# Kernel optimization log

Measured on AMD Instinct MI355X. Metric: run time of the kernel, lower is better.

The kernel has to match this reference:

```python
import jax, jax.numpy as jnp
import numpy as np
from jax import lax

B, T, C = 4, 1024, 1024
H, HEAD = 16, 64            # n_head, head size (K == V == HEAD)
TM_DIM, TD_DIM = 32, 64     # TIME_MIX_EXTRA_DIM, W_MIX_EXTRA_DIM
N_LAYER, LAYER_ID = 24, 12
EPS = 1e-5
HEAD_DIV = 8.0              # head_size_divisor


def setup_inputs() -> dict:
    key = jax.random.key(0)
    ks = jax.random.split(key, 10)
    r1 = 1.0 - LAYER_ID / N_LAYER          # ratio_1_to_almost0
    r0 = LAYER_ID / max(N_LAYER - 1, 1)    # ratio_0_to_1
    ddd = np.arange(C, dtype=np.float64) / C
    x_maa = (1.0 - ddd ** r1).astype(np.float32)
    r_maa = (1.0 - ddd ** (0.5 * r1)).astype(np.float32)
    v_maa = (1.0 - (ddd ** r1 + 0.3 * r0)).astype(np.float32)
    n = np.arange(H * HEAD, dtype=np.float64)
    denom = max(H * HEAD - 1, 1)
    time_decay = (-6.0 + 5.0 * (n / denom) ** (0.7 + 1.3 * r0)).reshape(H, HEAD).astype(np.float32)
    zig = (((np.arange(H * HEAD) + 1) % 3) - 1) * 0.1
    time_first = (r0 * (1.0 - n / denom) + zig).reshape(H, HEAD).astype(np.float32)

    def unif(k, shape, s=0.01):
        return jax.random.uniform(k, shape, jnp.float32, -s, s)

    return {
        "x": jax.random.normal(ks[0], (B, T, C), jnp.float32),
        "x_maa": jnp.asarray(x_maa),
        "w_maa": jnp.asarray(x_maa),
        "k_maa": jnp.asarray(x_maa),
        "v_maa": jnp.asarray(v_maa),
        "r_maa": jnp.asarray(r_maa),
        "g_maa": jnp.asarray(r_maa),
        "tm_w1": unif(ks[1], (C, 5 * TM_DIM)),
        "tm_w2": unif(ks[2], (5, TM_DIM, C)),
        "td_w1": unif(ks[3], (C, TD_DIM)),
        "td_w2": unif(ks[4], (TD_DIM, C)),
        "time_decay": jnp.asarray(time_decay),
        "time_first": jnp.asarray(time_first),
        "Wr": jax.random.normal(ks[5], (C, H * HEAD), jnp.float32) * 0.02,
        "Wk": jax.random.normal(ks[6], (C, H * HEAD), jnp.float32) * 0.02,
        "Wv": jax.random.normal(ks[7], (C, H * HEAD), jnp.float32) * 0.02,
        "Wg": jax.random.normal(ks[8], (C, H * HEAD), jnp.float32) * 0.02,
        "Wo": jax.random.normal(ks[9], (H * HEAD, C), jnp.float32) * 0.02,
        "ln_w": jnp.ones((H * HEAD,), jnp.float32),
        "ln_b": jnp.zeros((H * HEAD,), jnp.float32),
    }


def reference(x, x_maa, w_maa, k_maa, v_maa, r_maa, g_maa,
              tm_w1, tm_w2, td_w1, td_w2, time_decay, time_first,
              Wr, Wk, Wv, Wg, Wo, ln_w, ln_b):
    B, T, C = x.shape
    H, K = time_decay.shape
    V = Wv.shape[1] // H
    # token shift: sx = x_{t-1} - x_t (zero-padded at t=0)
    sx = jnp.concatenate([jnp.zeros_like(x[:, :1]), x[:, :-1]], axis=1) - x
    # data-dependent token-mix LoRA: 5 mixing deltas
    mix = jnp.tanh((x + sx * x_maa) @ tm_w1).reshape(B, T, 5, TM_DIM)
    mix = jnp.einsum('btfd,fdc->fbtc', mix, tm_w2)  # [5,B,T,C]
    mw, mk, mv, mr, mg = mix
    wx = x + sx * (w_maa + mw)
    kx = x + sx * (k_maa + mk)
    vx = x + sx * (v_maa + mv)
    rx = x + sx * (r_maa + mr)
    gx = x + sx * (g_maa + mg)
    r = (rx @ Wr).reshape(B, T, H, K)
    k = (kx @ Wk).reshape(B, T, H, K)
    v = (vx @ Wv).reshape(B, T, H, V)
    g = jax.nn.silu(gx @ Wg)                         # [B,T,H*V]
    # data-dependent decay via LoRA, then double-exp squash into (0,1)
    w = time_decay[None, None] + (jnp.tanh(wx @ td_w1) @ td_w2).reshape(B, T, H, K)
    w = jnp.exp(-jnp.exp(w))                         # [B,T,H,K]
    u = time_first                                   # [H,K]

    def step(s, inp):
        rt, kt, vt, wt = inp                         # [B,H,K],[B,H,K],[B,H,V],[B,H,K]
        kv = kt[..., None] * vt[..., None, :]        # [B,H,K,V] outer product
        y = jnp.einsum('bhk,bhkv->bhv', rt, s + u[None, :, :, None] * kv)
        return wt[..., None] * s + kv, y

    s0 = jnp.zeros((B, H, K, V), x.dtype)
    xs = (jnp.moveaxis(r, 1, 0), jnp.moveaxis(k, 1, 0),
          jnp.moveaxis(v, 1, 0), jnp.moveaxis(w, 1, 0))
    _, ys = lax.scan(step, s0, xs)                   # ys: [T,B,H,V]
    out = jnp.moveaxis(ys, 0, 1).reshape(B, T, H, V) / HEAD_DIV
    # GroupNorm with n_kv_head groups over dim_v channels -> per-head norm
    mu = out.mean(-1, keepdims=True)
    var = out.var(-1, keepdims=True)
    out = ((out - mu) * lax.rsqrt(var + EPS)).reshape(B, T, H * V) * ln_w + ln_b
    return (out * g) @ Wo
```

## Files before the change

kernel.cpp:

```cpp
#include <hip/hip_runtime.h>
#include <hip/hip_bf16.h>
#include <math.h>
#include <stdint.h>

constexpr int Bn = 4, Tn = 1024, Cn = 1024, Hn = 16;
constexpr int BT = Bn * Tn;
constexpr long long BTC = (long long)BT * Cn;
constexpr int CL = 64;
constexpr int NC = Tn / CL;

typedef __bf16 bf16x8_t __attribute__((ext_vector_type(8)));
typedef float f32x4_t __attribute__((ext_vector_type(4)));
typedef unsigned short us8_t __attribute__((ext_vector_type(8)));

__device__ __forceinline__ unsigned short f2bf_bits(float v) {
    __hip_bfloat16 h = __float2bfloat16(v);
    return *reinterpret_cast<unsigned short*>(&h);
}
__device__ __forceinline__ float bfbits2f(unsigned short u) {
    unsigned int x = (unsigned int)u << 16;
    return __uint_as_float(x);
}

__device__ __forceinline__ void gload16(const void* g, void* l) {
    auto const* gp = reinterpret_cast<const unsigned int __attribute__((address_space(1)))*>(
        reinterpret_cast<uintptr_t>(g));
    auto* lp = reinterpret_cast<unsigned int __attribute__((address_space(3)))*>(
        reinterpret_cast<uintptr_t>(l));
    __builtin_amdgcn_global_load_lds(gp, lp, 16, 0, 0);
}

__global__ __launch_bounds__(256) void transp8(const float* __restrict__ W0,
                                               const float* __restrict__ W1,
                                               const float* __restrict__ W2,
                                               const float* __restrict__ W3,
                                               const float* __restrict__ W4,
                                               const float* __restrict__ W5,
                                               const float* __restrict__ W6,
                                               const float* __restrict__ W7,
                                               __hip_bfloat16* __restrict__ T0,
                                               __hip_bfloat16* __restrict__ T1,
                                               __hip_bfloat16* __restrict__ T2,
                                               __hip_bfloat16* __restrict__ T3,
                                               __hip_bfloat16* __restrict__ T4,
                                               __hip_bfloat16* __restrict__ T5,
                                               __hip_bfloat16* __restrict__ T6,
                                               __hip_bfloat16* __restrict__ T7) {
    int z = blockIdx.z;
    const float* W;
    __hip_bfloat16* Wt;
    int R, Cc;
    if (z < 5) {
        W = (z == 0) ? W0 : (z == 1) ? W1 : (z == 2) ? W2 : (z == 3) ? W3 : W4;
        Wt = (z == 0) ? T0 : (z == 1) ? T1 : (z == 2) ? T2 : (z == 3) ? T3 : T4;
        R = Cn; Cc = Cn;
    } else if (z == 5) {
        if (blockIdx.x >= 5) return;
        W = W5; Wt = T5; R = Cn; Cc = 160;
    } else if (z == 6) {
        if (blockIdx.y >= 5) return;
        W = W6; Wt = T6; R = 160; Cc = Cn;
    } else {
        if (blockIdx.y >= 2) return;
        W = W7; Wt = T7; R = 64; Cc = Cn;
    }
    __shared__ float tile[32][33];
    int c0 = blockIdx.x * 32, r0 = blockIdx.y * 32;
    int tx = threadIdx.x & 31, ty = threadIdx.x >> 5;
    #pragma unroll
    for (int i = 0; i < 4; i++)
        tile[ty + 8 * i][tx] = W[(size_t)(r0 + ty + 8 * i) * Cc + c0 + tx];
    __syncthreads();
    #pragma unroll
    for (int i = 0; i < 4; i++)
        Wt[(size_t)(c0 + ty + 8 * i) * R + r0 + tx] = __float2bfloat16(tile[tx][ty + 8 * i]);
}

template <int KS>
__global__ __launch_bounds__(256) void gemm_f32_splitk(const float* __restrict__ A,
                                                       const float* __restrict__ Bm,
                                                       float* __restrict__ part,
                                                       int M, int N, int K) {
    __shared__ float As[16][64];
    __shared__ float Bs[16][64];
    int tid = threadIdx.x;
    int kp = blockIdx.x;
    int m0 = blockIdx.y * 64;
    int kbeg = kp * (K / KS), kend = kbeg + K / KS;
    int tx = tid & 15, ty = tid >> 4;
    int ar = tid >> 2, ac = (tid & 3) * 4;
    int br = tid >> 4, bc = (tid & 15) * 4;
    float acc[4][4] = {};

    for (int k0 = kbeg; k0 < kend; k0 += 16) {
        float4 av = *reinterpret_cast<const float4*>(A + (size_t)(m0 + ar) * K + k0 + ac);
        As[ac + 0][ar] = av.x; As[ac + 1][ar] = av.y;
        As[ac + 2][ar] = av.z; As[ac + 3][ar] = av.w;
        *reinterpret_cast<float4*>(&Bs[br][bc]) =
            *reinterpret_cast<const float4*>(Bm + (size_t)(k0 + br) * N + bc);
        __syncthreads();
        #pragma unroll
        for (int kk = 0; kk < 16; kk++) {
            float4 a4 = *reinterpret_cast<const float4*>(&As[kk][ty * 4]);
            float4 b4 = *reinterpret_cast<const float4*>(&Bs[kk][tx * 4]);
            float aa[4] = {a4.x, a4.y, a4.z, a4.w};
            float bb[4] = {b4.x, b4.y, b4.z, b4.w};
            #pragma unroll
            for (int i = 0; i < 4; i++)
                #pragma unroll
                for (int j = 0; j < 4; j++)
                    acc[i][j] = fmaf(aa[i], bb[j], acc[i][j]);
        }
        __syncthreads();
    }
    #pragma unroll
    for (int i = 0; i < 4; i++) {
        int row = m0 + ty * 4 + i;
        #pragma unroll
        for (int j = 0; j < 4; j++)
            part[((size_t)kp * M + row) * N + tx * 4 + j] = acc[i][j];
    }
}

template <int KS>
__global__ __launch_bounds__(256) void splitk_reduce_tanh_bf(const float* __restrict__ part,
                                                             __hip_bfloat16* __restrict__ outp,
                                                             int total, size_t stride) {
    int i = blockIdx.x * 256 + threadIdx.x;
    if (i >= total) return;
    float s = 0.f;
    #pragma unroll
    for (int kp = 0; kp < KS; kp++) s += part[kp * stride + i];
    outp[i] = __float2bfloat16(tanhf(s));
}

template <int KS>
__global__ __launch_bounds__(256) void gemm_mfma_sk(const float* __restrict__ x,
                                                    const float* __restrict__ x_maa,
                                                    const __hip_bfloat16* __restrict__ Bt,
                                                    float* __restrict__ part,
                                                    int M, int N, int K) {
    __shared__ alignas(16) unsigned short As[64 * 64];
    __shared__ alignas(16) unsigned short Bs[128 * 64];
    int tid = threadIdx.x;
    int m0 = blockIdx.y * 64, n0 = blockIdx.x * 128;
    int kp = blockIdx.z;
    int kbeg = kp * (K / KS), kend = kbeg + K / KS;
    int wave = tid >> 6, lane = tid & 63;
    int wm = (wave & 1) * 32, wn = (wave >> 1) * 64;
    int l15 = lane & 15, l4 = lane >> 4;
    f32x4_t acc[2][4] = {};

    for (int k0 = kbeg; k0 < kend; k0 += 64) {
        #pragma unroll
        for (int p = 0; p < 2; p++) {
            int cch = tid + p * 256;
            int row = cch >> 3, slot = cch & 7;
            int s2 = slot ^ (row & 7);
            int gr = m0 + row;
            int t = gr & (Tn - 1);
            size_t gx = (size_t)gr * Cn + k0 + slot * 8;
            float4 xa0 = *reinterpret_cast<const float4*>(x + gx);
            float4 xa1 = *reinterpret_cast<const float4*>(x + gx + 4);
            float4 xp0 = make_float4(0.f, 0.f, 0.f, 0.f), xp1 = xp0;
            if (t > 0) {
                xp0 = *reinterpret_cast<const float4*>(x + gx - Cn);
                xp1 = *reinterpret_cast<const float4*>(x + gx - Cn + 4);
            }
            float4 ma0 = *reinterpret_cast<const float4*>(x_maa + k0 + slot * 8);
            float4 ma1 = *reinterpret_cast<const float4*>(x_maa + k0 + slot * 8 + 4);
            ushort4 o0, o1;
            o0.x = f2bf_bits(xa0.x + (xp0.x - xa0.x) * ma0.x);
            o0.y = f2bf_bits(xa0.y + (xp0.y - xa0.y) * ma0.y);
            o0.z = f2bf_bits(xa0.z + (xp0.z - xa0.z) * ma0.z);
            o0.w = f2bf_bits(xa0.w + (xp0.w - xa0.w) * ma0.w);
            o1.x = f2bf_bits(xa1.x + (xp1.x - xa1.x) * ma1.x);
            o1.y = f2bf_bits(xa1.y + (xp1.y - xa1.y) * ma1.y);
            o1.z = f2bf_bits(xa1.z + (xp1.z - xa1.z) * ma1.z);
            o1.w = f2bf_bits(xa1.w + (xp1.w - xa1.w) * ma1.w);
            *reinterpret_cast<ushort4*>(&As[row * 64 + s2 * 8]) = o0;
            *reinterpret_cast<ushort4*>(&As[row * 64 + s2 * 8 + 4]) = o1;
        }
        #pragma unroll
        for (int p = 0; p < 4; p++) {
            int cch = tid + p * 256;
            int row = cch >> 3, slot = cch & 7;
            int s2 = slot ^ (row & 7);
            int rowg = n0 + row; if (rowg > N - 1) rowg = N - 1;
            *reinterpret_cast<us8_t*>(&Bs[row * 64 + s2 * 8]) =
                *reinterpret_cast<const us8_t*>(&Bt[(size_t)rowg * K + k0 + slot * 8]);
        }
        __syncthreads();
        #pragma unroll
        for (int kw = 0; kw < 2; kw++) {
            int slot = kw * 4 + l4;
            bf16x8_t af[2], bfr[4];
            #pragma unroll
            for (int f = 0; f < 2; f++) {
                int ar = wm + f * 16 + l15;
                af[f] = *reinterpret_cast<const bf16x8_t*>(&As[ar * 64 + (slot ^ (ar & 7)) * 8]);
            }
            #pragma unroll
            for (int f = 0; f < 4; f++) {
                int br = wn + f * 16 + l15;
                bfr[f] = *reinterpret_cast<const bf16x8_t*>(&Bs[br * 64 + (slot ^ (br & 7)) * 8]);
            }
            #pragma unroll
            for (int i = 0; i < 2; i++)
                #pragma unroll
                for (int j = 0; j < 4; j++)
                    acc[i][j] = __builtin_amdgcn_mfma_f32_16x16x32_bf16(af[i], bfr[j], acc[i][j], 0, 0, 0);
        }
        __syncthreads();
    }

    #pragma unroll
    for (int i = 0; i < 2; i++) {
        int rbase = m0 + wm + i * 16 + l4 * 4;
        #pragma unroll
        for (int j = 0; j < 4; j++) {
            int col = n0 + wn + j * 16 + l15;
            if (col < N) {
                #pragma unroll
                for (int q = 0; q < 4; q++)
                    part[((size_t)kp * M + rbase + q) * N + col] = acc[i][j][q];
            }
        }
    }
}

__global__ __launch_bounds__(256) void gemm_mfma_decay(const __hip_bfloat16* __restrict__ A,
                                                       const __hip_bfloat16* __restrict__ Bt,
                                                       const float* __restrict__ extra,
                                                       float* __restrict__ Cout,
                                                       int M, int N) {
    __shared__ alignas(16) unsigned short As[64 * 64];
    __shared__ alignas(16) unsigned short Bs[128 * 64];
    int tid = threadIdx.x;
    int m0 = blockIdx.x * 64, n0 = blockIdx.y * 128;
    int wave = tid >> 6, lane = tid & 63;
    int wm = (wave & 1) * 32, wn = (wave >> 1) * 64;
    int l15 = lane & 15, l4 = lane >> 4;
    int lrow = lane >> 3, ls2 = lane & 7;
    f32x4_t acc[2][4] = {};

    #pragma unroll
    for (int ci = 0; ci < 2; ci++) {
        int r0 = wave * 16 + ci * 8;
        int row = r0 + lrow;
        int gs = ls2 ^ (row & 7);
        gload16(&A[(size_t)(m0 + row) * 64 + gs * 8], &As[r0 * 64]);
    }
    #pragma unroll
    for (int ci = 0; ci < 4; ci++) {
        int r0 = wave * 32 + ci * 8;
        int row = r0 + lrow;
        int gs = ls2 ^ (row & 7);
        gload16(&Bt[(size_t)(n0 + row) * 64 + gs * 8], &Bs[r0 * 64]);
    }
    __syncthreads();
    #pragma unroll
    for (int kw = 0; kw < 2; kw++) {
        int slot = kw * 4 + l4;
        bf16x8_t af[2], bfr[4];
        #pragma unroll
        for (int f = 0; f < 2; f++) {
            int ar = wm + f * 16 + l15;
            af[f] = *reinterpret_cast<const bf16x8_t*>(&As[ar * 64 + (slot ^ (ar & 7)) * 8]);
        }
        #pragma unroll
        for (int f = 0; f < 4; f++) {
            int br = wn + f * 16 + l15;
            bfr[f] = *reinterpret_cast<const bf16x8_t*>(&Bs[br * 64 + (slot ^ (br & 7)) * 8]);
        }
        #pragma unroll
        for (int i = 0; i < 2; i++)
            #pragma unroll
            for (int j = 0; j < 4; j++)
                acc[i][j] = __builtin_amdgcn_mfma_f32_16x16x32_bf16(af[i], bfr[j], acc[i][j], 0, 0, 0);
    }

    #pragma unroll
    for (int i = 0; i < 2; i++) {
        int rbase = m0 + wm + i * 16 + l4 * 4;
        #pragma unroll
        for (int j = 0; j < 4; j++) {
            int col = n0 + wn + j * 16 + l15;
            float ex = extra[col];
            #pragma unroll
            for (int q = 0; q < 4; q++)
                Cout[(size_t)(rbase + q) * N + col] = -expf(ex + acc[i][j][q]);
        }
    }
}

__global__ __launch_bounds__(256) void dmix_gemm(const __hip_bfloat16* __restrict__ A,
                                                 const __hip_bfloat16* __restrict__ W2T,
                                                 const float* __restrict__ x,
                                                 const float* __restrict__ wmaa,
                                                 const float* __restrict__ kmaa,
                                                 const float* __restrict__ vmaa,
                                                 const float* __restrict__ rmaa,
                                                 const float* __restrict__ gmaa,
                                                 float* __restrict__ wx,
                                                 __hip_bfloat16* __restrict__ kxb,
                                                 __hip_bfloat16* __restrict__ vxb,
                                                 __hip_bfloat16* __restrict__ rxb,
                                                 __hip_bfloat16* __restrict__ gxb) {
    __shared__ alignas(16) unsigned short As[64 * 32];
    __shared__ alignas(16) unsigned short Bs[128 * 32];
    int tid = threadIdx.x;
    int m0 = blockIdx.x * 64, n0 = blockIdx.y * 128;
    int f  = blockIdx.z;
    int wave = tid >> 6, lane = tid & 63;
    int wm = (wave & 1) * 32, wn = (wave >> 1) * 64;
    int l15 = lane & 15, l4 = lane >> 4;
    int lrow2 = lane >> 2, ls = lane & 3;
    f32x4_t acc[2][4] = {};

    {
        int row = wave * 16 + lrow2;
        int gs = ls ^ (row & 3);
        gload16(&A[(size_t)(m0 + row) * 160 + f * 32 + gs * 8], &As[(wave * 16) * 32]);
    }
    #pragma unroll
    for (int ci = 0; ci < 2; ci++) {
        int r0 = wave * 32 + ci * 16;
        int row = r0 + lrow2;
        int gs = ls ^ (row & 3);
        gload16(&W2T[(size_t)(n0 + row) * 160 + f * 32 + gs * 8], &Bs[r0 * 32]);
    }
    __syncthreads();
    bf16x8_t af[2], bfr[4];
    #pragma unroll
    for (int i = 0; i < 2; i++) {
        int ar = wm + i * 16 + l15;
        af[i] = *reinterpret_cast<const bf16x8_t*>(&As[ar * 32 + ((l4 ^ (ar & 3)) * 8)]);
    }
    #pragma unroll
    for (int j = 0; j < 4; j++) {
        int br = wn + j * 16 + l15;
        bfr[j] = *reinterpret_cast<const bf16x8_t*>(&Bs[br * 32 + ((l4 ^ (br & 3)) * 8)]);
    }
    #pragma unroll
    for (int i = 0; i < 2; i++)
        #pragma unroll
        for (int j = 0; j < 4; j++)
            acc[i][j] = __builtin_amdgcn_mfma_f32_16x16x32_bf16(af[i], bfr[j], acc[i][j], 0, 0, 0);

    const float* maa = (f == 0) ? wmaa : (f == 1) ? kmaa : (f == 2) ? vmaa
                     : (f == 3) ? rmaa : gmaa;
    __hip_bfloat16* dstb = (f == 1) ? kxb : (f == 2) ? vxb : (f == 3) ? rxb : gxb;
    #pragma unroll
    for (int i = 0; i < 2; i++) {
        int rbase = m0 + wm + i * 16 + l4 * 4;
        #pragma unroll
        for (int j = 0; j < 4; j++) {
            int col = n0 + wn + j * 16 + l15;
            float mv = maa[col];
            #pragma unroll
            for (int q = 0; q < 4; q++) {
                int row = rbase + q;
                int t = row & (Tn - 1);
                size_t o = (size_t)row * Cn + col;
                float xv = x[o];
                float xp = (t > 0) ? x[o - Cn] : 0.f;
                float val = xv + (xp - xv) * (mv + acc[i][j][q]);
                if (f == 0) wx[o] = val;
                else        dstb[o] = __float2bfloat16(val);
            }
        }
    }
}

__global__ __launch_bounds__(256) void gemm_qkvg(const __hip_bfloat16* __restrict__ A0,
                                                 const __hip_bfloat16* __restrict__ A1,
                                                 const __hip_bfloat16* __restrict__ A2,
                                                 const __hip_bfloat16* __restrict__ A3,
                                                 const __hip_bfloat16* __restrict__ B0,
                                                 const __hip_bfloat16* __restrict__ B1,
                                                 const __hip_bfloat16* __restrict__ B2,
                                                 const __hip_bfloat16* __restrict__ B3,
                                                 __hip_bfloat16* __restrict__ C0,
                                                 __hip_bfloat16* __restrict__ C1,
                                                 __hip_bfloat16* __restrict__ C2,
                                                 __hip_bfloat16* __restrict__ C3,
                                                 int M, int N, int K) {
    int g = blockIdx.z;
    const __hip_bfloat16* A  = (g == 0) ? A0 : (g == 1) ? A1 : (g == 2) ? A2 : A3;
    const __hip_bfloat16* Bt = (g == 0) ? B0 : (g == 1) ? B1 : (g == 2) ? B2 : B3;
    __hip_bfloat16* Co = (g == 0) ? C0 : (g == 1) ? C1 : (g == 2) ? C2 : C3;
    __shared__ alignas(16) unsigned short As[64 * 64];
    __shared__ alignas(16) unsigned short Bs[128 * 64];
    int tid = threadIdx.x;
    int m0 = blockIdx.x * 64, n0 = blockIdx.y * 128;
    int wave = tid >> 6, lane = tid & 63;
    int wm = (wave & 1) * 32, wn = (wave >> 1) * 64;
    int l15 = lane & 15, l4 = lane >> 4;
    int lrow = lane >> 3, ls2 = lane & 7;
    f32x4_t acc[2][4] = {};

    for (int k0 = 0; k0 < K; k0 += 64) {
        #pragma unroll
        for (int ci = 0; ci < 2; ci++) {
            int r0 = wave * 16 + ci * 8;
            int row = r0 + lrow;
            int gs = ls2 ^ (row & 7);
            gload16(&A[(size_t)(m0 + row) * K + k0 + gs * 8], &As[r0 * 64]);
        }
        #pragma unroll
        for (int ci = 0; ci < 4; ci++) {
            int r0 = wave * 32 + ci * 8;
            int row = r0 + lrow;
            int gs = ls2 ^ (row & 7);
            gload16(&Bt[(size_t)(n0 + row) * K + k0 + gs * 8], &Bs[r0 * 64]);
        }
        __syncthreads();
        #pragma unroll
        for (int kw = 0; kw < 2; kw++) {
            int slot = kw * 4 + l4;
            bf16x8_t af[2], bfr[4];
            #pragma unroll
            for (int f = 0; f < 2; f++) {
                int ar = wm + f * 16 + l15;
                af[f] = *reinterpret_cast<const bf16x8_t*>(&As[ar * 64 + (slot ^ (ar & 7)) * 8]);
            }
            #pragma unroll
            for (int f = 0; f < 4; f++) {
                int br = wn + f * 16 + l15;
                bfr[f] = *reinterpret_cast<const bf16x8_t*>(&Bs[br * 64 + (slot ^ (br & 7)) * 8]);
            }
            #pragma unroll
            for (int i = 0; i < 2; i++)
                #pragma unroll
                for (int j = 0; j < 4; j++)
                    acc[i][j] = __builtin_amdgcn_mfma_f32_16x16x32_bf16(af[i], bfr[j], acc[i][j], 0, 0, 0);
        }
        __syncthreads();
    }

    #pragma unroll
    for (int i = 0; i < 2; i++) {
        int rbase = m0 + wm + i * 16 + l4 * 4;
        #pragma unroll
        for (int j = 0; j < 4; j++) {
            int col = n0 + wn + j * 16 + l15;
            #pragma unroll
            for (int q = 0; q < 4; q++) {
                float v = acc[i][j][q];
                if (g == 3) v = v / (1.f + expf(-v));
                Co[(size_t)(rbase + q) * N + col] = __float2bfloat16(v);
            }
        }
    }
}

__global__ __launch_bounds__(256) void gemm_mfma_gl(const __hip_bfloat16* __restrict__ A,
                                                    const __hip_bfloat16* __restrict__ Bt,
                                                    float* __restrict__ Cout,
                                                    int M, int N, int K) {
    __shared__ alignas(16) unsigned short As[64 * 64];
    __shared__ alignas(16) unsigned short Bs[128 * 64];
    int tid = threadIdx.x;
    int m0 = blockIdx.x * 64, n0 = blockIdx.y * 128;
    int wave = tid >> 6, lane = tid & 63;
    int wm = (wave & 1) * 32, wn = (wave >> 1) * 64;
    int l15 = lane & 15, l4 = lane >> 4;
    int lrow = lane >> 3, ls2 = lane & 7;
    f32x4_t acc[2][4] = {};

    for (int k0 = 0; k0 < K; k0 += 64) {
        #pragma unroll
        for (int ci = 0; ci < 2; ci++) {
            int r0 = wave * 16 + ci * 8;
            int row = r0 + lrow;
            int gs = ls2 ^ (row & 7);
            gload16(&A[(size_t)(m0 + row) * K + k0 + gs * 8], &As[r0 * 64]);
        }
        #pragma unroll
        for (int ci = 0; ci < 4; ci++) {
            int r0 = wave * 32 + ci * 8;
            int row = r0 + lrow;
            int gs = ls2 ^ (row & 7);
            gload16(&Bt[(size_t)(n0 + row) * K + k0 + gs * 8], &Bs[r0 * 64]);
        }
        __syncthreads();
        #pragma unroll
        for (int kw = 0; kw < 2; kw++) {
            int slot = kw * 4 + l4;
            bf16x8_t af[2], bfr[4];
            #pragma unroll
            for (int f = 0; f < 2; f++) {
                int ar = wm + f * 16 + l15;
                af[f] = *reinterpret_cast<const bf16x8_t*>(&As[ar * 64 + (slot ^ (ar & 7)) * 8]);
            }
            #pragma unroll
            for (int f = 0; f < 4; f++) {
                int br = wn + f * 16 + l15;
                bfr[f] = *reinterpret_cast<const bf16x8_t*>(&Bs[br * 64 + (slot ^ (br & 7)) * 8]);
            }
            #pragma unroll
            for (int i = 0; i < 2; i++)
                #pragma unroll
                for (int j = 0; j < 4; j++)
                    acc[i][j] = __builtin_amdgcn_mfma_f32_16x16x32_bf16(af[i], bfr[j], acc[i][j], 0, 0, 0);
        }
        __syncthreads();
    }

    #pragma unroll
    for (int i = 0; i < 2; i++) {
        int rbase = m0 + wm + i * 16 + l4 * 4;
        #pragma unroll
        for (int j = 0; j < 4; j++) {
            int col = n0 + wn + j * 16 + l15;
            #pragma unroll
            for (int q = 0; q < 4; q++)
                Cout[(size_t)(rbase + q) * N + col] = acc[i][j][q];
        }
    }
}

__global__ __launch_bounds__(256) void chunk_summary(const __hip_bfloat16* __restrict__ kb,
                                                     const __hip_bfloat16* __restrict__ vb,
                                                     const float* __restrict__ lw,
                                                     __hip_bfloat16* __restrict__ Bc,
                                                     float* __restrict__ Wtot) {
    int bid = blockIdx.x;
    int c = bid & 15, h = (bid >> 4) & 15, b = bid >> 8;
    size_t gbase = ((size_t)(b * Tn + c * CL) * Hn + h) * 64;
    int tid = threadIdx.x;
    __shared__ float linc[64][68];
    __shared__ float wtp[4][64];
    __shared__ alignas(16) __hip_bfloat16 kdT[64][72];
    __shared__ alignas(16) __hip_bfloat16 vsT[64][72];
    int wave = tid >> 6, lane = tid & 63;
    {
        float acc = 0.f;
        #pragma unroll
        for (int i = 0; i < 16; i++) {
            int t = wave * 16 + i;
            acc += lw[gbase + (size_t)t * 1024 + lane];
            linc[t][lane] = acc;
        }
        wtp[wave][lane] = acc;
    }
    __syncthreads();
    {
        float off = 0.f;
        for (int g = 0; g < wave; g++) off += wtp[g][lane];
        #pragma unroll
        for (int i = 0; i < 16; i++) linc[wave * 16 + i][lane] += off;
    }
    __syncthreads();
    int t4 = tid >> 2, c0 = (tid & 3) * 16;
    #pragma unroll
    for (int i = 0; i < 4; i++) {
        int ch = c0 + i * 4;
        size_t ga = gbase + (size_t)t4 * 1024 + ch;
        ushort4 ku = *reinterpret_cast<const ushort4*>(kb + ga);
        ushort4 vu = *reinterpret_cast<const ushort4*>(vb + ga);
        float kk[4] = {bfbits2f(ku.x), bfbits2f(ku.y), bfbits2f(ku.z), bfbits2f(ku.w)};
        float vv[4] = {bfbits2f(vu.x), bfbits2f(vu.y), bfbits2f(vu.z), bfbits2f(vu.w)};
        #pragma unroll
        for (int j = 0; j < 4; j++) {
            float li = linc[t4][ch + j];
            float lend = linc[63][ch + j];
            kdT[ch + j][t4] = __float2bfloat16(kk[j] * expf(lend - li));
            vsT[ch + j][t4] = __float2bfloat16(vv[j]);
        }
    }
    if (tid < 64) Wtot[(size_t)bid * 64 + tid] = expf(linc[63][tid]);
    __syncthreads();
    int l15 = lane & 15, l4q = lane >> 4;
    #pragma unroll
    for (int nt = 0; nt < 4; nt++) {
        f32x4_t acc = {};
        #pragma unroll
        for (int kt = 0; kt < 2; kt++) {
            bf16x8_t a = *reinterpret_cast<const bf16x8_t*>(&kdT[wave * 16 + l15][kt * 32 + l4q * 8]);
            bf16x8_t bb = *reinterpret_cast<const bf16x8_t*>(&vsT[nt * 16 + l15][kt * 32 + l4q * 8]);
            acc = __builtin_amdgcn_mfma_f32_16x16x32_bf16(a, bb, acc, 0, 0, 0);
        }
        #pragma unroll
        for (int q = 0; q < 4; q++) {
            int krow = wave * 16 + l4q * 4 + q;
            Bc[(size_t)bid * 4096 + (size_t)krow * 64 + nt * 16 + l15] = __float2bfloat16(acc[q]);
        }
    }
}

__global__ __launch_bounds__(256) void chunk_scan(const __hip_bfloat16* __restrict__ Bc,
                                                  const float* __restrict__ Wtot,
                                                  __hip_bfloat16* __restrict__ SbufT) {
    int bid = blockIdx.x;
    int bh = bid >> 2, vg = bid & 3;
    int kk = threadIdx.x >> 2;
    int v = vg * 16 + (threadIdx.x & 3) * 4;
    float4 S = make_float4(0.f, 0.f, 0.f, 0.f);
    for (int c = 0; c < NC; c++) {
        size_t base = (size_t)(bh * NC + c) * 4096;
        SbufT[base + (size_t)(v + 0) * 64 + kk] = __float2bfloat16(S.x);
        SbufT[base + (size_t)(v + 1) * 64 + kk] = __float2bfloat16(S.y);
        SbufT[base + (size_t)(v + 2) * 64 + kk] = __float2bfloat16(S.z);
        SbufT[base + (size_t)(v + 3) * 64 + kk] = __float2bfloat16(S.w);
        float wt = Wtot[(size_t)(bh * NC + c) * 64 + kk];
        ushort4 b4 = *reinterpret_cast<const ushort4*>(Bc + base + (size_t)kk * 64 + v);
        S.x = fmaf(wt, S.x, bfbits2f(b4.x));
        S.y = fmaf(wt, S.y, bfbits2f(b4.y));
        S.z = fmaf(wt, S.z, bfbits2f(b4.z));
        S.w = fmaf(wt, S.w, bfbits2f(b4.w));
    }
}

__global__ __launch_bounds__(256) void chunk_out(const __hip_bfloat16* __restrict__ rb,
                                                 const __hip_bfloat16* __restrict__ kb,
                                                 const __hip_bfloat16* __restrict__ vb,
                                                 const float* __restrict__ lw,
                                                 const __hip_bfloat16* __restrict__ SbufT,
                                                 const float* __restrict__ tf,
                                                 const __hip_bfloat16* __restrict__ gb,
                                                 const float* __restrict__ lnw,
                                                 const float* __restrict__ lnb,
                                                 __hip_bfloat16* __restrict__ fin) {
    int bid = blockIdx.x;
    int c = bid & 15, h = (bid >> 4) & 15, b = bid >> 8;
    size_t gbase = ((size_t)(b * Tn + c * CL) * Hn + h) * 64;
    int tid = threadIdx.x;
    __shared__ alignas(16) __hip_bfloat16 qs[64][72];
    __shared__ alignas(16) __hip_bfloat16 ks[64][72];
    __shared__ alignas(16) __hip_bfloat16 vsT[64][72];
    __shared__ alignas(16) __hip_bfloat16 scT[64][72];
    __shared__ alignas(16) float uni[64 * 68];
    __shared__ float wtp[4][64];
    __shared__ float diag[64];
    float (*linc)[68] = reinterpret_cast<float(*)[68]>(uni);
    __hip_bfloat16 (*asb)[72] = reinterpret_cast<__hip_bfloat16(*)[72]>(uni);
    int wave = tid >> 6, lane = tid & 63;
    {
        float acc = 0.f;
        #pragma unroll
        for (int i = 0; i < 16; i++) {
            int t = wave * 16 + i;
            acc += lw[gbase + (size_t)t * 1024 + lane];
            linc[t][lane] = acc;
        }
        wtp[wave][lane] = acc;
    }
    __syncthreads();
    {
        float off = 0.f;
        for (int g = 0; g < wave; g++) off += wtp[g][lane];
        #pragma unroll
        for (int i = 0; i < 16; i++) linc[wave * 16 + i][lane] += off;
    }
    __syncthreads();
    int t4 = tid >> 2, c0 = (tid & 3) * 16;
    float dpart = 0.f;
    #pragma unroll
    for (int i = 0; i < 4; i++) {
        int ch = c0 + i * 4;
        size_t ga = gbase + (size_t)t4 * 1024 + ch;
        ushort4 ru = *reinterpret_cast<const ushort4*>(rb + ga);
        ushort4 ku = *reinterpret_cast<const ushort4*>(kb + ga);
        ushort4 vu = *reinterpret_cast<const ushort4*>(vb + ga);
        float4 l4v = *reinterpret_cast<const float4*>(lw + ga);
        float4 u4 = *reinterpret_cast<const float4*>(tf + h * 64 + ch);
        ushort4 s4 = *reinterpret_cast<const ushort4*>(SbufT + (size_t)bid * 4096 + (size_t)t4 * 64 + ch);
        float rr[4] = {bfbits2f(ru.x), bfbits2f(ru.y), bfbits2f(ru.z), bfbits2f(ru.w)};
        float kkv[4] = {bfbits2f(ku.x), bfbits2f(ku.y), bfbits2f(ku.z), bfbits2f(ku.w)};
        float vv[4] = {bfbits2f(vu.x), bfbits2f(vu.y), bfbits2f(vu.z), bfbits2f(vu.w)};
        float lwv[4] = {l4v.x, l4v.y, l4v.z, l4v.w};
        float uu[4] = {u4.x, u4.y, u4.z, u4.w};
        unsigned short ssb[4] = {s4.x, s4.y, s4.z, s4.w};
        #pragma unroll
        for (int j = 0; j < 4; j++) {
            float li = linc[t4][ch + j];
            qs[t4][ch + j] = __float2bfloat16(rr[j] * expf(li - lwv[j]));
            ks[t4][ch + j] = __float2bfloat16(kkv[j] * expf(-li));
            vsT[ch + j][t4] = __float2bfloat16(vv[j]);
            *reinterpret_cast<unsigned short*>(&scT[t4][ch + j]) = ssb[j];
            dpart = fmaf(rr[j] * uu[j], kkv[j], dpart);
        }
    }
    dpart += __shfl_xor(dpart, 1);
    dpart += __shfl_xor(dpart, 2);
    if ((tid & 3) == 0) diag[t4] = dpart;
    __syncthreads();
    int l15 = lane & 15, l4q = lane >> 4;
    #pragma unroll
    for (int nt = 0; nt < 4; nt++) {
        f32x4_t acc = {};
        if (nt <= wave) {
            #pragma unroll
            for (int kt = 0; kt < 2; kt++) {
                bf16x8_t a = *reinterpret_cast<const bf16x8_t*>(&qs[wave * 16 + l15][kt * 32 + l4q * 8]);
                bf16x8_t bb = *reinterpret_cast<const bf16x8_t*>(&ks[nt * 16 + l15][kt * 32 + l4q * 8]);
                acc = __builtin_amdgcn_mfma_f32_16x16x32_bf16(a, bb, acc, 0, 0, 0);
            }
        }
        #pragma unroll
        for (int q = 0; q < 4; q++) {
            int t = wave * 16 + l4q * 4 + q;
            int tau = nt * 16 + l15;
            float v = (tau < t) ? acc[q] : (tau == t ? diag[t] : 0.f);
            asb[t][tau] = __float2bfloat16(v);
        }
    }
    __syncthreads();
    f32x4_t oacc[4];
    #pragma unroll
    for (int nt = 0; nt < 4; nt++) {
        f32x4_t acc = {};
        int kmax = (wave >> 1) + 1;
        for (int kt = 0; kt < kmax; kt++) {
            bf16x8_t a = *reinterpret_cast<const bf16x8_t*>(&asb[wave * 16 + l15][kt * 32 + l4q * 8]);
            bf16x8_t bb = *reinterpret_cast<const bf16x8_t*>(&vsT[nt * 16 + l15][kt * 32 + l4q * 8]);
            acc = __builtin_amdgcn_mfma_f32_16x16x32_bf16(a, bb, acc, 0, 0, 0);
        }
        #pragma unroll
        for (int kt = 0; kt < 2; kt++) {
            bf16x8_t a = *reinterpret_cast<const bf16x8_t*>(&qs[wave * 16 + l15][kt * 32 + l4q * 8]);
            bf16x8_t bb = *reinterpret_cast<const bf16x8_t*>(&scT[nt * 16 + l15][kt * 32 + l4q * 8]);
            acc = __builtin_amdgcn_mfma_f32_16x16x32_bf16(a, bb, acc, 0, 0, 0);
        }
        oacc[nt] = acc;
    }
    float sum[4] = {0.f, 0.f, 0.f, 0.f}, sq[4] = {0.f, 0.f, 0.f, 0.f};
    #pragma unroll
    for (int nt = 0; nt < 4; nt++)
        #pragma unroll
        for (int q = 0; q < 4; q++) {
            float v = oacc[nt][q] * 0.125f;
            oacc[nt][q] = v;
            sum[q] += v;
            sq[q] += v * v;
        }
    #pragma unroll
    for (int off = 1; off < 16; off <<= 1)
        #pragma unroll
        for (int q = 0; q < 4; q++) {
            sum[q] += __shfl_xor(sum[q], off, 64);
            sq[q]  += __shfl_xor(sq[q],  off, 64);
        }
    float mu[4], rs[4];
    #pragma unroll
    for (int q = 0; q < 4; q++) {
        mu[q] = sum[q] * (1.f / 64.f);
        float var = sq[q] * (1.f / 64.f) - mu[q] * mu[q];
        rs[q] = rsqrtf(var + 1e-5f);
    }
    #pragma unroll
    for (int nt = 0; nt < 4; nt++) {
        int v = nt * 16 + l15;
        float lw_ = lnw[h * 64 + v];
        float lb_ = lnb[h * 64 + v];
        #pragma unroll
        for (int q = 0; q < 4; q++) {
            int t = wave * 16 + l4q * 4 + q;
            size_t o = gbase + (size_t)t * 1024 + v;
            float gv = bfbits2f(*reinterpret_cast<const unsigned short*>(&gb[o]));
            float val = (oacc[nt][q] - mu[q]) * rs[q] * lw_ + lb_;
            fin[o] = __float2bfloat16(val * gv);
        }
    }
}

extern "C" void kernel_launch(void* const* d_in, const int* in_sizes, int n_in,
                              void* d_out, int out_size, void* d_ws, size_t ws_size,
                              hipStream_t stream) {
    (void)in_sizes; (void)n_in; (void)out_size; (void)ws_size;
    const float* x      = (const float*)d_in[0];
    const float* x_maa  = (const float*)d_in[1];
    const float* w_maa  = (const float*)d_in[2];
    const float* k_maa  = (const float*)d_in[3];
    const float* v_maa  = (const float*)d_in[4];
    const float* r_maa  = (const float*)d_in[5];
    const float* g_maa  = (const float*)d_in[6];
    const float* tm_w1  = (const float*)d_in[7];
    const float* tm_w2  = (const float*)d_in[8];
    const float* td_w1  = (const float*)d_in[9];
    const float* td_w2  = (const float*)d_in[10];
    const float* t_dec  = (const float*)d_in[11];
    const float* t_first= (const float*)d_in[12];
    const float* Wr     = (const float*)d_in[13];
    const float* Wk     = (const float*)d_in[14];
    const float* Wv     = (const float*)d_in[15];
    const float* Wg     = (const float*)d_in[16];
    const float* Wo     = (const float*)d_in[17];
    const float* ln_w   = (const float*)d_in[18];
    const float* ln_b   = (const float*)d_in[19];
    float* out = (float*)d_out;

    char* ws = (char*)d_ws;
    size_t off = 0;
    auto alloc = [&](size_t bytes) -> void* {
        void* p = ws + off;
        off = (off + bytes + 255) & ~(size_t)255;
        return p;
    };
    __hip_bfloat16* rb = (__hip_bfloat16*)alloc(BTC * 2);
    __hip_bfloat16* mix160b = (__hip_bfloat16*)alloc((size_t)BT * 160 * 2);
    float* wxr    = (float*)alloc(BTC * 4);
    __hip_bfloat16* kxb = (__hip_bfloat16*)alloc(BTC * 2);
    __hip_bfloat16* vxb = (__hip_bfloat16*)alloc(BTC * 2);
    __hip_bfloat16* rxb = (__hip_bfloat16*)alloc(BTC * 2);
    __hip_bfloat16* gxb = (__hip_bfloat16*)alloc(BTC * 2);
    __hip_bfloat16* kb  = (__hip_bfloat16*)alloc(BTC * 2);
    __hip_bfloat16* vb  = (__hip_bfloat16*)alloc(BTC * 2);
    __hip_bfloat16* gb  = (__hip_bfloat16*)alloc(BTC * 2);
    float* wl1 = (float*)alloc((size_t)BT * 64 * 4);
    float* lwb = (float*)alloc(BTC * 4);
    __hip_bfloat16* WrT = (__hip_bfloat16*)alloc((size_t)Cn * Cn * 2);
    __hip_bfloat16* WkT = (__hip_bfloat16*)alloc((size_t)Cn * Cn * 2);
    __hip_bfloat16* WvT = (__hip_bfloat16*)alloc((size_t)Cn * Cn * 2);
    __hip_bfloat16* WgT = (__hip_bfloat16*)alloc((size_t)Cn * Cn * 2);
    __hip_bfloat16* WoT = (__hip_bfloat16*)alloc((size_t)Cn * Cn * 2);
    __hip_bfloat16* tmw1T = (__hip_bfloat16*)alloc((size_t)160 * Cn * 2);
    __hip_bfloat16* w2T   = (__hip_bfloat16*)alloc((size_t)Cn * 160 * 2);
    __hip_bfloat16* tdw2T = (__hip_bfloat16*)alloc((size_t)Cn * 64 * 2);
    __hip_bfloat16* wl1b  = (__hip_bfloat16*)alloc((size_t)BT * 64 * 2);
    float* WtB = (float*)alloc((size_t)Bn * Hn * NC * 64 * 4);
    char* big = (char*)alloc((size_t)4 * BT * 160 * 4);
    float* lorapart = (float*)big;
    float* skpart = (float*)big;
    (void)wl1;
    __hip_bfloat16* BcB = (__hip_bfloat16*)wxr;
    __hip_bfloat16* SbufT = rxb;
    __hip_bfloat16* fin = kxb;

    dim3 blk(256);
    transp8<<<dim3(32, 32, 8), blk, 0, stream>>>(Wr, Wk, Wv, Wg, Wo, tm_w1, tm_w2, td_w2,
                                                 WrT, WkT, WvT, WgT, WoT, tmw1T, w2T, tdw2T);
    gemm_mfma_sk<4><<<dim3(2, 64, 4), blk, 0, stream>>>(x, x_maa, tmw1T, lorapart, BT, 160, Cn);
    splitk_reduce_tanh_bf<4><<<dim3((BT * 160 + 255) / 256), blk, 0, stream>>>(
        lorapart, mix160b, BT * 160, (size_t)BT * 160);
    dmix_gemm<<<dim3(64, 8, 5), blk, 0, stream>>>(mix160b, w2T, x,
                                                  w_maa, k_maa, v_maa, r_maa, g_maa,
                                                  wxr, kxb, vxb, rxb, gxb);
    gemm_qkvg<<<dim3(64, 8, 4), blk, 0, stream>>>(rxb, kxb, vxb, gxb,
                                                  WrT, WkT, WvT, WgT,
                                                  rb, kb, vb, gb, BT, Cn, Cn);
    gemm_f32_splitk<8><<<dim3(8, 64), blk, 0, stream>>>(wxr, td_w1, skpart, BT, 64, Cn);
    splitk_reduce_tanh_bf<8><<<dim3(BT * 64 / 256), blk, 0, stream>>>(skpart, wl1b, BT * 64,
                                                                      (size_t)BT * 64);
    gemm_mfma_decay<<<dim3(64, 8), blk, 0, stream>>>(wl1b, tdw2T, t_dec, lwb, BT, Cn);
    chunk_summary<<<dim3(Bn * Hn * NC), blk, 0, stream>>>(kb, vb, lwb, BcB, WtB);
    chunk_scan<<<dim3(Bn * Hn * 4), blk, 0, stream>>>(BcB, WtB, SbufT);
    chunk_out<<<dim3(Bn * Hn * NC), blk, 0, stream>>>(rb, kb, vb, lwb, SbufT, t_first,
                                                      gb, ln_w, ln_b, fin);
    gemm_mfma_gl<<<dim3(64, 8), blk, 0, stream>>>(fin, WoT, out, BT, Cn, Cn);
}
```

Before: 184.3 us.

## Fuse decay LoRA GEMM into chunk_summary and chunk_out kernels

Removes the standalone decay GEMM, which wrote a BxTxC fp32 log-decay tensor that was then read twice. Each chunk kernel now computes its own 64x64 decay tile with MFMA directly from the bf16 LoRA activations and transposed weights, writes it into LDS and prefix-sums it there. chunk_out now takes the exclusive prefix from the previous LDS row instead of subtracting the per-step value. This saves a launch and about 16MB of fp32 write plus two reads, at the cost of doing the small decay GEMM twice and reading the A and B fragments uncached from global memory.

```diff
diff --git a/kernel.cpp b/kernel.cpp
--- a/kernel.cpp
+++ b/kernel.cpp
@@ -229,71 +229,6 @@
     }
 }
 
-__global__ __launch_bounds__(256) void gemm_mfma_decay(const __hip_bfloat16* __restrict__ A,
-                                                       const __hip_bfloat16* __restrict__ Bt,
-                                                       const float* __restrict__ extra,
-                                                       float* __restrict__ Cout,
-                                                       int M, int N) {
-    __shared__ alignas(16) unsigned short As[64 * 64];
-    __shared__ alignas(16) unsigned short Bs[128 * 64];
-    int tid = threadIdx.x;
-    int m0 = blockIdx.x * 64, n0 = blockIdx.y * 128;
-    int wave = tid >> 6, lane = tid & 63;
-    int wm = (wave & 1) * 32, wn = (wave >> 1) * 64;
-    int l15 = lane & 15, l4 = lane >> 4;
-    int lrow = lane >> 3, ls2 = lane & 7;
-    f32x4_t acc[2][4] = {};
-
-    #pragma unroll
-    for (int ci = 0; ci < 2; ci++) {
-        int r0 = wave * 16 + ci * 8;
-        int row = r0 + lrow;
-        int gs = ls2 ^ (row & 7);
-        gload16(&A[(size_t)(m0 + row) * 64 + gs * 8], &As[r0 * 64]);
-    }
-    #pragma unroll
-    for (int ci = 0; ci < 4; ci++) {
-        int r0 = wave * 32 + ci * 8;
-        int row = r0 + lrow;
-        int gs = ls2 ^ (row & 7);
-        gload16(&Bt[(size_t)(n0 + row) * 64 + gs * 8], &Bs[r0 * 64]);
-    }
-    __syncthreads();
-    #pragma unroll
-    for (int kw = 0; kw < 2; kw++) {
-        int slot = kw * 4 + l4;
-        bf16x8_t af[2], bfr[4];
-        #pragma unroll
-        for (int f = 0; f < 2; f++) {
-            int ar = wm + f * 16 + l15;
-            af[f] = *reinterpret_cast<const bf16x8_t*>(&As[ar * 64 + (slot ^ (ar & 7)) * 8]);
-        }
-        #pragma unroll
-        for (int f = 0; f < 4; f++) {
-            int br = wn + f * 16 + l15;
-            bfr[f] = *reinterpret_cast<const bf16x8_t*>(&Bs[br * 64 + (slot ^ (br & 7)) * 8]);
-        }
-        #pragma unroll
-        for (int i = 0; i < 2; i++)
-            #pragma unroll
-            for (int j = 0; j < 4; j++)
-                acc[i][j] = __builtin_amdgcn_mfma_f32_16x16x32_bf16(af[i], bfr[j], acc[i][j], 0, 0, 0);
-    }
-
-    #pragma unroll
-    for (int i = 0; i < 2; i++) {
-        int rbase = m0 + wm + i * 16 + l4 * 4;
-        #pragma unroll
-        for (int j = 0; j < 4; j++) {
-            int col = n0 + wn + j * 16 + l15;
-            float ex = extra[col];
-            #pragma unroll
-            for (int q = 0; q < 4; q++)
-                Cout[(size_t)(rbase + q) * N + col] = -expf(ex + acc[i][j][q]);
-        }
-    }
-}
-
 __global__ __launch_bounds__(256) void dmix_gemm(const __hip_bfloat16* __restrict__ A,
                                                  const __hip_bfloat16* __restrict__ W2T,
                                                  const float* __restrict__ x,
@@ -521,37 +456,71 @@
     }
 }
 
+__device__ __forceinline__ void decay_tile(const __hip_bfloat16* __restrict__ wl1b,
+                                           const __hip_bfloat16* __restrict__ tdw2T,
+                                           const float* __restrict__ t_dec,
+                                           int h, size_t row0,
+                                           float linc[64][68],
+                                           int wave, int lane) {
+    int l15 = lane & 15, l4 = lane >> 4;
+    #pragma unroll
+    for (int nt = 0; nt < 4; nt++) {
+        f32x4_t acc = {};
+        #pragma unroll
+        for (int kw = 0; kw < 2; kw++) {
+            int arow = row0 + wave * 16 + l15;
+            bf16x8_t a = *reinterpret_cast<const bf16x8_t*>(
+                &wl1b[(size_t)arow * 64 + (kw * 4 + l4) * 8]);
+            int bcol = h * 64 + nt * 16 + l15;
+            bf16x8_t b = *reinterpret_cast<const bf16x8_t*>(
+                &tdw2T[(size_t)bcol * 64 + (kw * 4 + l4) * 8]);
+            acc = __builtin_amdgcn_mfma_f32_16x16x32_bf16(a, b, acc, 0, 0, 0);
+        }
+        #pragma unroll
+        for (int q = 0; q < 4; q++) {
+            int t = wave * 16 + l4 * 4 + q;
+            int ch = nt * 16 + l15;
+            linc[t][ch] = -expf(t_dec[h * 64 + ch] + acc[q]);
+        }
+    }
+}
+
+__device__ __forceinline__ void prefix_lds(float linc[64][68], float wtp[4][64],
+                                           int wave, int lane) {
+    float acc = 0.f;
+    #pragma unroll
+    for (int i = 0; i < 16; i++) {
+        acc += linc[wave * 16 + i][lane];
+        linc[wave * 16 + i][lane] = acc;
+    }
+    wtp[wave][lane] = acc;
+    __syncthreads();
+    float off = 0.f;
+    for (int g = 0; g < wave; g++) off += wtp[g][lane];
+    #pragma unroll
+    for (int i = 0; i < 16; i++) linc[wave * 16 + i][lane] += off;
+}
+
 __global__ __launch_bounds__(256) void chunk_summary(const __hip_bfloat16* __restrict__ kb,
                                                      const __hip_bfloat16* __restrict__ vb,
-                                                     const float* __restrict__ lw,
+                                                     const __hip_bfloat16* __restrict__ wl1b,
+                                                     const __hip_bfloat16* __restrict__ tdw2T,
+                                                     const float* __restrict__ t_dec,
                                                      __hip_bfloat16* __restrict__ Bc,
                                                      float* __restrict__ Wtot) {
     int bid = blockIdx.x;
     int c = bid & 15, h = (bid >> 4) & 15, b = bid >> 8;
-    size_t gbase = ((size_t)(b * Tn + c * CL) * Hn + h) * 64;
+    size_t row0 = (size_t)(b * Tn + c * CL);
+    size_t gbase = row0 * Cn + (size_t)h * 64;
     int tid = threadIdx.x;
     __shared__ float linc[64][68];
     __shared__ float wtp[4][64];
     __shared__ alignas(16) __hip_bfloat16 kdT[64][72];
     __shared__ alignas(16) __hip_bfloat16 vsT[64][72];
     int wave = tid >> 6, lane = tid & 63;
-    {
-        float acc = 0.f;
-        #pragma unroll
-        for (int i = 0; i < 16; i++) {
-            int t = wave * 16 + i;
-            acc += lw[gbase + (size_t)t * 1024 + lane];
-            linc[t][lane] = acc;
-        }
-        wtp[wave][lane] = acc;
-    }
-    __syncthreads();
-    {
-        float off = 0.f;
-        for (int g = 0; g < wave; g++) off += wtp[g][lane];
-        #pragma unroll
-        for (int i = 0; i < 16; i++) linc[wave * 16 + i][lane] += off;
-    }
+    decay_tile(wl1b, tdw2T, t_dec, h, row0, linc, wave, lane);
+    __syncthreads();
+    prefix_lds(linc, wtp, wave, lane);
     __syncthreads();
     int t4 = tid >> 2, c0 = (tid & 3) * 16;
     #pragma unroll
@@ -616,7 +585,9 @@
 __global__ __launch_bounds__(256) void chunk_out(const __hip_bfloat16* __restrict__ rb,
                                                  const __hip_bfloat16* __restrict__ kb,
                                                  const __hip_bfloat16* __restrict__ vb,
-                                                 const float* __restrict__ lw,
+                                                 const __hip_bfloat16* __restrict__ wl1b,
+                                                 const __hip_bfloat16* __restrict__ tdw2T,
+                                                 const float* __restrict__ t_dec,
                                                  const __hip_bfloat16* __restrict__ SbufT,
                                                  const float* __restrict__ tf,
                                                  const __hip_bfloat16* __restrict__ gb,
@@ -625,7 +596,8 @@
                                                  __hip_bfloat16* __restrict__ fin) {
     int bid = blockIdx.x;
     int c = bid & 15, h = (bid >> 4) & 15, b = bid >> 8;
-    size_t gbase = ((size_t)(b * Tn + c * CL) * Hn + h) * 64;
+    size_t row0 = (size_t)(b * Tn + c * CL);
+    size_t gbase = row0 * Cn + (size_t)h * 64;
     int tid = threadIdx.x;
     __shared__ alignas(16) __hip_bfloat16 qs[64][72];
     __shared__ alignas(16) __hip_bfloat16 ks[64][72];
@@ -637,23 +609,9 @@
     float (*linc)[68] = reinterpret_cast<float(*)[68]>(uni);
     __hip_bfloat16 (*asb)[72] = reinterpret_cast<__hip_bfloat16(*)[72]>(uni);
     int wave = tid >> 6, lane = tid & 63;
-    {
-        float acc = 0.f;
-        #pragma unroll
-        for (int i = 0; i < 16; i++) {
-            int t = wave * 16 + i;
-            acc += lw[gbase + (size_t)t * 1024 + lane];
-            linc[t][lane] = acc;
-        }
-        wtp[wave][lane] = acc;
-    }
-    __syncthreads();
-    {
-        float off = 0.f;
-        for (int g = 0; g < wave; g++) off += wtp[g][lane];
-        #pragma unroll
-        for (int i = 0; i < 16; i++) linc[wave * 16 + i][lane] += off;
-    }
+    decay_tile(wl1b, tdw2T, t_dec, h, row0, linc, wave, lane);
+    __syncthreads();
+    prefix_lds(linc, wtp, wave, lane);
     __syncthreads();
     int t4 = tid >> 2, c0 = (tid & 3) * 16;
     float dpart = 0.f;
@@ -664,19 +622,18 @@
         ushort4 ru = *reinterpret_cast<const ushort4*>(rb + ga);
         ushort4 ku = *reinterpret_cast<const ushort4*>(kb + ga);
         ushort4 vu = *reinterpret_cast<const ushort4*>(vb + ga);
-        float4 l4v = *reinterpret_cast<const float4*>(lw + ga);
         float4 u4 = *reinterpret_cast<const float4*>(tf + h * 64 + ch);
         ushort4 s4 = *reinterpret_cast<const ushort4*>(SbufT + (size_t)bid * 4096 + (size_t)t4 * 64 + ch);
         float rr[4] = {bfbits2f(ru.x), bfbits2f(ru.y), bfbits2f(ru.z), bfbits2f(ru.w)};
         float kkv[4] = {bfbits2f(ku.x), bfbits2f(ku.y), bfbits2f(ku.z), bfbits2f(ku.w)};
         float vv[4] = {bfbits2f(vu.x), bfbits2f(vu.y), bfbits2f(vu.z), bfbits2f(vu.w)};
-        float lwv[4] = {l4v.x, l4v.y, l4v.z, l4v.w};
         float uu[4] = {u4.x, u4.y, u4.z, u4.w};
         unsigned short ssb[4] = {s4.x, s4.y, s4.z, s4.w};
         #pragma unroll
         for (int j = 0; j < 4; j++) {
             float li = linc[t4][ch + j];
-            qs[t4][ch + j] = __float2bfloat16(rr[j] * expf(li - lwv[j]));
+            float lex = (t4 > 0) ? linc[t4 - 1][ch + j] : 0.f;
+            qs[t4][ch + j] = __float2bfloat16(rr[j] * expf(lex));
             ks[t4][ch + j] = __float2bfloat16(kkv[j] * expf(-li));
             vsT[ch + j][t4] = __float2bfloat16(vv[j]);
             *reinterpret_cast<unsigned short*>(&scT[t4][ch + j]) = ssb[j];
@@ -809,8 +766,6 @@
     __hip_bfloat16* kb  = (__hip_bfloat16*)alloc(BTC * 2);
     __hip_bfloat16* vb  = (__hip_bfloat16*)alloc(BTC * 2);
     __hip_bfloat16* gb  = (__hip_bfloat16*)alloc(BTC * 2);
-    float* wl1 = (float*)alloc((size_t)BT * 64 * 4);
-    float* lwb = (float*)alloc(BTC * 4);
     __hip_bfloat16* WrT = (__hip_bfloat16*)alloc((size_t)Cn * Cn * 2);
     __hip_bfloat16* WkT = (__hip_bfloat16*)alloc((size_t)Cn * Cn * 2);
     __hip_bfloat16* WvT = (__hip_bfloat16*)alloc((size_t)Cn * Cn * 2);
@@ -824,7 +779,6 @@
     char* big = (char*)alloc((size_t)4 * BT * 160 * 4);
     float* lorapart = (float*)big;
     float* skpart = (float*)big;
-    (void)wl1;
     __hip_bfloat16* BcB = (__hip_bfloat16*)wxr;
     __hip_bfloat16* SbufT = rxb;
     __hip_bfloat16* fin = kxb;
@@ -844,10 +798,9 @@
     gemm_f32_splitk<8><<<dim3(8, 64), blk, 0, stream>>>(wxr, td_w1, skpart, BT, 64, Cn);
     splitk_reduce_tanh_bf<8><<<dim3(BT * 64 / 256), blk, 0, stream>>>(skpart, wl1b, BT * 64,
                                                                       (size_t)BT * 64);
-    gemm_mfma_decay<<<dim3(64, 8), blk, 0, stream>>>(wl1b, tdw2T, t_dec, lwb, BT, Cn);
-    chunk_summary<<<dim3(Bn * Hn * NC), blk, 0, stream>>>(kb, vb, lwb, BcB, WtB);
+    chunk_summary<<<dim3(Bn * Hn * NC), blk, 0, stream>>>(kb, vb, wl1b, tdw2T, t_dec, BcB, WtB);
     chunk_scan<<<dim3(Bn * Hn * 4), blk, 0, stream>>>(BcB, WtB, SbufT);
-    chunk_out<<<dim3(Bn * Hn * NC), blk, 0, stream>>>(rb, kb, vb, lwb, SbufT, t_first,
-                                                      gb, ln_w, ln_b, fin);
+    chunk_out<<<dim3(Bn * Hn * NC), blk, 0, stream>>>(rb, kb, vb, wl1b, tdw2T, t_dec,
+                                                      SbufT, t_first, gb, ln_w, ln_b, fin);
     gemm_mfma_gl<<<dim3(64, 8), blk, 0, stream>>>(fin, WoT, out, BT, Cn, Cn);
 }
```

After: 186.9 us. About the same (+1.4%).
